# Performance work log

Measured on AMD Instinct MI355X. Metric: run time of the kernel, lower is better.

The kernel has to match this reference:

```python
import jax, jax.numpy as jnp
import numpy as np

EPS = 1e-8  # matches torch F.cosine_similarity eps


def setup_inputs() -> dict:
    key = jax.random.key(0)
    k1, = jax.random.split(key, 1)
    N, U, D = 512, 32, 512
    embeddings = jax.random.normal(k1, (N, U, D), dtype=jnp.float32)
    w = jnp.asarray(10.0, dtype=jnp.float32)  # init_w
    b = jnp.asarray(-5.0, dtype=jnp.float32)  # init_b
    return {"embeddings": embeddings, "w": w, "b": b}


def reference(embeddings, w, b):
    N, U, D = embeddings.shape
    # centroids per speaker (mean over utterances; module includes current utt)
    centroids = embeddings.mean(axis=1)  # (N, D)
    # cosine similarity via normalize + matmul
    e = embeddings.reshape(N * U, D)
    e_n = e / jnp.maximum(jnp.linalg.norm(e, axis=-1, keepdims=True), EPS)
    c_n = centroids / jnp.maximum(
        jnp.linalg.norm(centroids, axis=-1, keepdims=True), EPS)
    sim = (e_n @ c_n.T).reshape(N, U, N)  # (N, U, N)
    sim = w * sim + b
    logp = jax.nn.log_softmax(sim, axis=-1)  # (N, U, N)
    # pick logp[j, k, j] for every j, k
    diag = jnp.take_along_axis(
        logp, jnp.arange(N)[:, None, None], axis=2)[..., 0]  # (N, U)
    return -diag.mean()
```

## Files before the change

kernel.cpp:

```cpp
#include <hip/hip_runtime.h>
#include <math.h>

#define N_SPK 512
#define N_UTT 32
#define DIM   512
#define EPSN  1e-8f

typedef __attribute__((ext_vector_type(8))) short  short8;
typedef __attribute__((ext_vector_type(4))) float  f32x4;

__device__ inline unsigned short f2bf(float x) {
  unsigned int u = __builtin_bit_cast(unsigned int, x);
  unsigned int r = (u + 0x7fffu + ((u >> 16) & 1u)) >> 16;
  return (unsigned short)r;
}

#define CNK_ELEMS (N_SPK * DIM)

__global__ __launch_bounds__(256) void centroid_kernel(
    const float* __restrict__ emb, unsigned short* __restrict__ cnk) {
  int j = blockIdx.x, t = threadIdx.x;
  int c4 = t & 127, half = t >> 7;
  const float4* base = (const float4*)(emb + (size_t)j * N_UTT * DIM);
  float4 s = {0.f, 0.f, 0.f, 0.f};
#pragma unroll
  for (int u = 0; u < 16; ++u) {
    float4 v = base[(half + 2 * u) * 128 + c4];
    s.x += v.x; s.y += v.y; s.z += v.z; s.w += v.w;
  }
  __shared__ float4 comb[128];
  if (half) comb[c4] = s;
  __syncthreads();
  float4 m = {0.f, 0.f, 0.f, 0.f};
  float ss = 0.f;
  if (!half) {
    float4 o = comb[c4];
    m.x = (s.x + o.x) * (1.f / N_UTT);
    m.y = (s.y + o.y) * (1.f / N_UTT);
    m.z = (s.z + o.z) * (1.f / N_UTT);
    m.w = (s.w + o.w) * (1.f / N_UTT);
    ss = m.x * m.x + m.y * m.y + m.z * m.z + m.w * m.w;
  }
#pragma unroll
  for (int off = 32; off > 0; off >>= 1) ss += __shfl_xor(ss, off, 64);
  __shared__ float red[4];
  if ((t & 63) == 0) red[t >> 6] = ss;
  __syncthreads();
  float total = red[0] + red[1] + red[2] + red[3];
  float inv = 1.f / fmaxf(sqrtf(total), EPSN);
  if (!half) {
    int d0 = c4 * 4;
    int kc = d0 >> 5;
    unsigned short* p = cnk + ((size_t)kc * N_SPK + j) * 32 + (d0 & 31);
    p[0] = f2bf(m.x * inv); p[1] = f2bf(m.y * inv);
    p[2] = f2bf(m.z * inv); p[3] = f2bf(m.w * inv);
  }
}

__global__ __launch_bounds__(512, 4) void ge2e_kernel(
    const float* __restrict__ emb, const unsigned short* __restrict__ cnk,
    const float* __restrict__ wp, const float* __restrict__ bp,
    float* __restrict__ partials) {
  __shared__ __align__(16) unsigned short E[N_UTT * DIM];
  __shared__ float red[8][N_UTT][2];
  __shared__ float dred[8];

  int j = blockIdx.x;
  int t = threadIdx.x;
  int lane = t & 63, wid = t >> 6;
  int n15 = lane & 15, quad = lane >> 4;

#pragma unroll
  for (int r8 = 0; r8 < 4; ++r8) {
    int r = wid * 4 + r8;
    const float* rp = emb + ((size_t)j * N_UTT + r) * DIM + lane * 8;
    float4 v0 = *(const float4*)rp;
    float4 v1 = *(const float4*)(rp + 4);
    float ss = v0.x * v0.x + v0.y * v0.y + v0.z * v0.z + v0.w * v0.w +
               v1.x * v1.x + v1.y * v1.y + v1.z * v1.z + v1.w * v1.w;
#pragma unroll
    for (int off = 32; off > 0; off >>= 1) ss += __shfl_xor(ss, off, 64);
    float inv = 1.f / fmaxf(sqrtf(ss), EPSN);
    short8 pk;
    pk[0] = (short)f2bf(v0.x * inv); pk[1] = (short)f2bf(v0.y * inv);
    pk[2] = (short)f2bf(v0.z * inv); pk[3] = (short)f2bf(v0.w * inv);
    pk[4] = (short)f2bf(v1.x * inv); pk[5] = (short)f2bf(v1.y * inv);
    pk[6] = (short)f2bf(v1.z * inv); pk[7] = (short)f2bf(v1.w * inv);
    int sw = lane ^ (r & 7);
    *(short8*)&E[r * DIM + sw * 8] = pk;
  }
  __syncthreads();

  f32x4 acc[2][4];
#pragma unroll
  for (int mt = 0; mt < 2; ++mt)
#pragma unroll
    for (int nt = 0; nt < 4; ++nt) acc[mt][nt] = (f32x4){0.f, 0.f, 0.f, 0.f};

  for (int ks = 0; ks < 16; ++ks) {
    short8 b[4];
#pragma unroll
    for (int nt = 0; nt < 4; ++nt) {
      int c = wid * 64 + nt * 16 + n15;
      b[nt] = *(const short8*)(cnk + ((size_t)ks * N_SPK + c) * 32 + quad * 8);
    }
    short8 a[2];
#pragma unroll
    for (int mt = 0; mt < 2; ++mt) {
      int r = mt * 16 + n15;
      int sw = (ks * 4 + quad) ^ (r & 7);
      a[mt] = *(const short8*)&E[r * DIM + sw * 8];
    }
#pragma unroll
    for (int mt = 0; mt < 2; ++mt)
#pragma unroll
      for (int nt = 0; nt < 4; ++nt)
        acc[mt][nt] = __builtin_amdgcn_mfma_f32_16x16x32_bf16(
            a[mt], b[nt], acc[mt][nt], 0, 0, 0);
  }

  float w = *wp, bb = *bp;
  float dsum = 0.f;
#pragma unroll
  for (int mt = 0; mt < 2; ++mt)
#pragma unroll
    for (int nt = 0; nt < 4; ++nt) {
      int c = wid * 64 + nt * 16 + n15;
      bool isdiag = (c == j);
#pragma unroll
      for (int rg = 0; rg < 4; ++rg) {
        float v = fmaf(w, acc[mt][nt][rg], bb);
        acc[mt][nt][rg] = v;
        if (isdiag) dsum += v;
      }
    }

#pragma unroll
  for (int mt = 0; mt < 2; ++mt)
#pragma unroll
    for (int rg = 0; rg < 4; ++rg) {
      float m = -INFINITY;
#pragma unroll
      for (int nt = 0; nt < 4; ++nt) m = fmaxf(m, acc[mt][nt][rg]);
#pragma unroll
      for (int off = 1; off < 16; off <<= 1) m = fmaxf(m, __shfl_xor(m, off, 64));
      float s = 0.f;
#pragma unroll
      for (int nt = 0; nt < 4; ++nt) s += __expf(acc[mt][nt][rg] - m);
#pragma unroll
      for (int off = 1; off < 16; off <<= 1) s += __shfl_xor(s, off, 64);
      if (n15 == 0) {
        int r = mt * 16 + quad * 4 + rg;
        red[wid][r][0] = m;
        red[wid][r][1] = s;
      }
    }
#pragma unroll
  for (int off = 32; off > 0; off >>= 1) dsum += __shfl_xor(dsum, off, 64);
  if (lane == 0) dred[wid] = dsum;
  __syncthreads();

  if (t < 32) {
    float M = -INFINITY;
#pragma unroll
    for (int ww = 0; ww < 8; ++ww) M = fmaxf(M, red[ww][t][0]);
    float S = 0.f;
#pragma unroll
    for (int ww = 0; ww < 8; ++ww) S += red[ww][t][1] * __expf(red[ww][t][0] - M);
    float lse = M + __logf(S);
#pragma unroll
    for (int off = 16; off > 0; off >>= 1) lse += __shfl_xor(lse, off, 64);
    if (t == 0) {
      float d = dred[0] + dred[1] + dred[2] + dred[3] +
                dred[4] + dred[5] + dred[6] + dred[7];
      partials[j] = lse - d;
    }
  }
}

__global__ __launch_bounds__(512) void finalize_kernel(
    const float* __restrict__ partials, float* __restrict__ out) {
  int t = threadIdx.x;
  float v = partials[t];
#pragma unroll
  for (int off = 32; off > 0; off >>= 1) v += __shfl_xor(v, off, 64);
  __shared__ float r[8];
  if ((t & 63) == 0) r[t >> 6] = v;
  __syncthreads();
  if (t == 0) {
    float s = r[0] + r[1] + r[2] + r[3] + r[4] + r[5] + r[6] + r[7];
    out[0] = s * (1.f / (N_SPK * N_UTT));
  }
}

extern "C" void kernel_launch(void* const* d_in, const int* in_sizes, int n_in,
                              void* d_out, int out_size, void* d_ws, size_t ws_size,
                              hipStream_t stream) {
  const float* emb = (const float*)d_in[0];
  const float* wp  = (const float*)d_in[1];
  const float* bp  = (const float*)d_in[2];
  float* out = (float*)d_out;
  unsigned short* cnk = (unsigned short*)d_ws;
  float* partials = (float*)((char*)d_ws + (size_t)CNK_ELEMS * 2);

  centroid_kernel<<<N_SPK, 256, 0, stream>>>(emb, cnk);
  ge2e_kernel<<<N_SPK, 512, 0, stream>>>(emb, cnk, wp, bp, partials);
  finalize_kernel<<<1, 512, 0, stream>>>(partials, out);
}
```

Baseline: 98.80 us.

## Fuse centroid and similarity kernels into one cooperative kernel with grid sync

Replaces the separate centroid and GE2E kernels with one cooperative kernel of 256 blocks of 1024 threads, each handling two speakers. The centroids are computed from the embeddings already loaded for normalization, so the second global read of the embeddings and one launch go away, and a grid-wide sync is used before the matmul. Each block now computes a 64x512 tile, which reuses every centroid fragment over twice as many rows. The cost is grid-sync overhead and only 256 resident blocks, with a fallback to the old three-kernel path if the cooperative launch fails.

```diff
diff --git a/kernel.cpp b/kernel.cpp
--- a/kernel.cpp
+++ b/kernel.cpp
@@ -1,10 +1,15 @@
 #include <hip/hip_runtime.h>
+#include <hip/hip_cooperative_groups.h>
 #include <math.h>
+
+namespace cg = cooperative_groups;
 
 #define N_SPK 512
 #define N_UTT 32
 #define DIM   512
 #define EPSN  1e-8f
+#define NBLK  256
+#define NTHR  1024
 
 typedef __attribute__((ext_vector_type(8))) short  short8;
 typedef __attribute__((ext_vector_type(4))) float  f32x4;
@@ -16,6 +21,182 @@
 }
 
 #define CNK_ELEMS (N_SPK * DIM)
+
+__global__ __launch_bounds__(NTHR) void ge2e_fused(
+    const float* __restrict__ emb, unsigned short* __restrict__ cnk,
+    const float* __restrict__ wp, const float* __restrict__ bp,
+    float* __restrict__ partials) {
+  __shared__ __align__(16) unsigned short E[64 * DIM];
+  __shared__ __align__(16) float part[14][DIM];
+  __shared__ float red[16][64][2];
+  __shared__ float dred[16];
+
+  int b = blockIdx.x;
+  int t = threadIdx.x;
+  int lane = t & 63, wid = t >> 6;
+  int n15 = lane & 15, quad = lane >> 4;
+  int sp = wid >> 3, ws8 = wid & 7;
+  int j = 2 * b + sp;
+
+  float4 v0[4], v1[4];
+  const float* base = emb + ((size_t)j * N_UTT + ws8 * 4) * DIM + lane * 8;
+#pragma unroll
+  for (int r4 = 0; r4 < 4; ++r4) {
+    v0[r4] = *(const float4*)(base + r4 * DIM);
+    v1[r4] = *(const float4*)(base + r4 * DIM + 4);
+  }
+  float cen[8] = {0.f, 0.f, 0.f, 0.f, 0.f, 0.f, 0.f, 0.f};
+#pragma unroll
+  for (int r4 = 0; r4 < 4; ++r4) {
+    cen[0] += v0[r4].x; cen[1] += v0[r4].y; cen[2] += v0[r4].z; cen[3] += v0[r4].w;
+    cen[4] += v1[r4].x; cen[5] += v1[r4].y; cen[6] += v1[r4].z; cen[7] += v1[r4].w;
+    float ss = v0[r4].x * v0[r4].x + v0[r4].y * v0[r4].y +
+               v0[r4].z * v0[r4].z + v0[r4].w * v0[r4].w +
+               v1[r4].x * v1[r4].x + v1[r4].y * v1[r4].y +
+               v1[r4].z * v1[r4].z + v1[r4].w * v1[r4].w;
+#pragma unroll
+    for (int off = 32; off > 0; off >>= 1) ss += __shfl_xor(ss, off, 64);
+    float inv = 1.f / fmaxf(sqrtf(ss), EPSN);
+    short8 pk;
+    pk[0] = (short)f2bf(v0[r4].x * inv); pk[1] = (short)f2bf(v0[r4].y * inv);
+    pk[2] = (short)f2bf(v0[r4].z * inv); pk[3] = (short)f2bf(v0[r4].w * inv);
+    pk[4] = (short)f2bf(v1[r4].x * inv); pk[5] = (short)f2bf(v1[r4].y * inv);
+    pk[6] = (short)f2bf(v1[r4].z * inv); pk[7] = (short)f2bf(v1[r4].w * inv);
+    int R = sp * 32 + ws8 * 4 + r4;
+    int sw = lane ^ (R & 7);
+    *(short8*)&E[R * DIM + sw * 8] = pk;
+  }
+  if (ws8 != 0) {
+    float* p = &part[sp * 7 + ws8 - 1][lane * 8];
+    *(float4*)p       = (float4){cen[0], cen[1], cen[2], cen[3]};
+    *(float4*)(p + 4) = (float4){cen[4], cen[5], cen[6], cen[7]};
+  }
+  __syncthreads();
+  if (ws8 == 0) {
+#pragma unroll
+    for (int i = 0; i < 7; ++i) {
+      const float* p = &part[sp * 7 + i][lane * 8];
+      float4 a = *(const float4*)p, c = *(const float4*)(p + 4);
+      cen[0] += a.x; cen[1] += a.y; cen[2] += a.z; cen[3] += a.w;
+      cen[4] += c.x; cen[5] += c.y; cen[6] += c.z; cen[7] += c.w;
+    }
+    float ss = 0.f;
+#pragma unroll
+    for (int k = 0; k < 8; ++k) {
+      cen[k] *= (1.f / N_UTT);
+      ss += cen[k] * cen[k];
+    }
+#pragma unroll
+    for (int off = 32; off > 0; off >>= 1) ss += __shfl_xor(ss, off, 64);
+    float inv = 1.f / fmaxf(sqrtf(ss), EPSN);
+    int kc = lane >> 2, ko = (lane & 3) * 8;
+    short8 pk;
+#pragma unroll
+    for (int k = 0; k < 8; ++k) pk[k] = (short)f2bf(cen[k] * inv);
+    *(short8*)(cnk + ((size_t)kc * N_SPK + j) * 32 + ko) = pk;
+  }
+  __threadfence();
+  cg::this_grid().sync();
+
+  f32x4 acc[4][2];
+#pragma unroll
+  for (int mt = 0; mt < 4; ++mt)
+#pragma unroll
+    for (int nt = 0; nt < 2; ++nt) acc[mt][nt] = (f32x4){0.f, 0.f, 0.f, 0.f};
+
+#pragma unroll 4
+  for (int ks = 0; ks < 16; ++ks) {
+    short8 bfr[2];
+#pragma unroll
+    for (int nt = 0; nt < 2; ++nt) {
+      int c = wid * 32 + nt * 16 + n15;
+      bfr[nt] = *(const short8*)(cnk + ((size_t)ks * N_SPK + c) * 32 + quad * 8);
+    }
+    short8 afr[4];
+#pragma unroll
+    for (int mt = 0; mt < 4; ++mt) {
+      int r = mt * 16 + n15;
+      int sw = (ks * 4 + quad) ^ (r & 7);
+      afr[mt] = *(const short8*)&E[r * DIM + sw * 8];
+    }
+#pragma unroll
+    for (int mt = 0; mt < 4; ++mt)
+#pragma unroll
+      for (int nt = 0; nt < 2; ++nt)
+        acc[mt][nt] = __builtin_amdgcn_mfma_f32_16x16x32_bf16(
+            afr[mt], bfr[nt], acc[mt][nt], 0, 0, 0);
+  }
+
+  float w = *wp, bb = *bp;
+  float dsum = 0.f;
+#pragma unroll
+  for (int mt = 0; mt < 4; ++mt)
+#pragma unroll
+    for (int nt = 0; nt < 2; ++nt) {
+      int c = wid * 32 + nt * 16 + n15;
+      bool isdiag = (c == 2 * b + (mt >> 1));
+#pragma unroll
+      for (int rg = 0; rg < 4; ++rg) {
+        float v = fmaf(w, acc[mt][nt][rg], bb);
+        acc[mt][nt][rg] = v;
+        if (isdiag) dsum += v;
+      }
+    }
+
+#pragma unroll
+  for (int mt = 0; mt < 4; ++mt)
+#pragma unroll
+    for (int rg = 0; rg < 4; ++rg) {
+      float m = fmaxf(acc[mt][0][rg], acc[mt][1][rg]);
+#pragma unroll
+      for (int off = 1; off < 16; off <<= 1) m = fmaxf(m, __shfl_xor(m, off, 64));
+      float s = __expf(acc[mt][0][rg] - m) + __expf(acc[mt][1][rg] - m);
+#pragma unroll
+      for (int off = 1; off < 16; off <<= 1) s += __shfl_xor(s, off, 64);
+      if (n15 == 0) {
+        int r = mt * 16 + quad * 4 + rg;
+        red[wid][r][0] = m;
+        red[wid][r][1] = s;
+      }
+    }
+#pragma unroll
+  for (int off = 32; off > 0; off >>= 1) dsum += __shfl_xor(dsum, off, 64);
+  if (lane == 0) dred[wid] = dsum;
+  __syncthreads();
+
+  if (t < 64) {
+    float M = -INFINITY;
+#pragma unroll
+    for (int ww = 0; ww < 16; ++ww) M = fmaxf(M, red[ww][t][0]);
+    float S = 0.f;
+#pragma unroll
+    for (int ww = 0; ww < 16; ++ww) S += red[ww][t][1] * __expf(red[ww][t][0] - M);
+    float lse = M + __logf(S);
+#pragma unroll
+    for (int off = 32; off > 0; off >>= 1) lse += __shfl_xor(lse, off, 64);
+    if (t == 0) {
+      float d = 0.f;
+#pragma unroll
+      for (int ww = 0; ww < 16; ++ww) d += dred[ww];
+      partials[b] = lse - d;
+    }
+  }
+}
+
+__global__ __launch_bounds__(512) void finalize_kernel(
+    const float* __restrict__ partials, float* __restrict__ out, int n) {
+  int t = threadIdx.x;
+  float v = (t < n) ? partials[t] : 0.f;
+#pragma unroll
+  for (int off = 32; off > 0; off >>= 1) v += __shfl_xor(v, off, 64);
+  __shared__ float r[8];
+  if ((t & 63) == 0) r[t >> 6] = v;
+  __syncthreads();
+  if (t == 0) {
+    float s = r[0] + r[1] + r[2] + r[3] + r[4] + r[5] + r[6] + r[7];
+    out[0] = s * (1.f / (N_SPK * N_UTT));
+  }
+}
 
 __global__ __launch_bounds__(256) void centroid_kernel(
     const float* __restrict__ emb, unsigned short* __restrict__ cnk) {
@@ -98,25 +279,25 @@
     for (int nt = 0; nt < 4; ++nt) acc[mt][nt] = (f32x4){0.f, 0.f, 0.f, 0.f};
 
   for (int ks = 0; ks < 16; ++ks) {
-    short8 b[4];
+    short8 bf[4];
 #pragma unroll
     for (int nt = 0; nt < 4; ++nt) {
       int c = wid * 64 + nt * 16 + n15;
-      b[nt] = *(const short8*)(cnk + ((size_t)ks * N_SPK + c) * 32 + quad * 8);
-    }
-    short8 a[2];
+      bf[nt] = *(const short8*)(cnk + ((size_t)ks * N_SPK + c) * 32 + quad * 8);
+    }
+    short8 af[2];
 #pragma unroll
     for (int mt = 0; mt < 2; ++mt) {
       int r = mt * 16 + n15;
       int sw = (ks * 4 + quad) ^ (r & 7);
-      a[mt] = *(const short8*)&E[r * DIM + sw * 8];
+      af[mt] = *(const short8*)&E[r * DIM + sw * 8];
     }
 #pragma unroll
     for (int mt = 0; mt < 2; ++mt)
 #pragma unroll
       for (int nt = 0; nt < 4; ++nt)
         acc[mt][nt] = __builtin_amdgcn_mfma_f32_16x16x32_bf16(
-            a[mt], b[nt], acc[mt][nt], 0, 0, 0);
+            af[mt], bf[nt], acc[mt][nt], 0, 0, 0);
   }
 
   float w = *wp, bb = *bp;
@@ -175,21 +356,6 @@
                 dred[4] + dred[5] + dred[6] + dred[7];
       partials[j] = lse - d;
     }
-  }
-}
-
-__global__ __launch_bounds__(512) void finalize_kernel(
-    const float* __restrict__ partials, float* __restrict__ out) {
-  int t = threadIdx.x;
-  float v = partials[t];
-#pragma unroll
-  for (int off = 32; off > 0; off >>= 1) v += __shfl_xor(v, off, 64);
-  __shared__ float r[8];
-  if ((t & 63) == 0) r[t >> 6] = v;
-  __syncthreads();
-  if (t == 0) {
-    float s = r[0] + r[1] + r[2] + r[3] + r[4] + r[5] + r[6] + r[7];
-    out[0] = s * (1.f / (N_SPK * N_UTT));
   }
 }
 
@@ -203,7 +369,15 @@
   unsigned short* cnk = (unsigned short*)d_ws;
   float* partials = (float*)((char*)d_ws + (size_t)CNK_ELEMS * 2);
 
-  centroid_kernel<<<N_SPK, 256, 0, stream>>>(emb, cnk);
-  ge2e_kernel<<<N_SPK, 512, 0, stream>>>(emb, cnk, wp, bp, partials);
-  finalize_kernel<<<1, 512, 0, stream>>>(partials, out);
-}
+  void* args[] = {(void*)&emb, (void*)&cnk, (void*)&wp, (void*)&bp,
+                  (void*)&partials};
+  hipError_t err = hipLaunchCooperativeKernel(
+      (const void*)ge2e_fused, dim3(NBLK), dim3(NTHR), args, 0, stream);
+  if (err == hipSuccess) {
+    finalize_kernel<<<1, 512, 0, stream>>>(partials, out, NBLK);
+  } else {
+    centroid_kernel<<<N_SPK, 256, 0, stream>>>(emb, cnk);
+    ge2e_kernel<<<N_SPK, 512, 0, stream>>>(emb, cnk, wp, bp, partials);
+    finalize_kernel<<<1, 512, 0, stream>>>(partials, out, N_SPK);
+  }
+}
```

New measurement: 193.9 us. +96.3%, slower.

## Process two speakers per block to halve centroid fragment reloads

Applied to the files above, without the earlier changes.

Each ge2e block now handles two speakers (64 rows) with 1024 threads, and every wave covers 32 centroid columns and 4 row tiles instead of 64 columns and 2 row tiles. Each centroid fragment loaded from global memory is reused across twice as many rows, so total centroid traffic drops by half. The trade-off is 256 blocks instead of 512, which on a large GPU may leave compute units idle, plus twice the LDS per block, which lowers occupancy. The finalize kernel is shrunk to match the 256 partials.

```diff
diff --git a/kernel.cpp b/kernel.cpp
--- a/kernel.cpp
+++ b/kernel.cpp
@@ -57,23 +57,25 @@
   }
 }
 
-__global__ __launch_bounds__(512, 4) void ge2e_kernel(
+__global__ __launch_bounds__(1024) void ge2e_kernel(
     const float* __restrict__ emb, const unsigned short* __restrict__ cnk,
     const float* __restrict__ wp, const float* __restrict__ bp,
     float* __restrict__ partials) {
-  __shared__ __align__(16) unsigned short E[N_UTT * DIM];
-  __shared__ float red[8][N_UTT][2];
-  __shared__ float dred[8];
-
-  int j = blockIdx.x;
+  __shared__ __align__(16) unsigned short E[64 * DIM];
+  __shared__ float red[16][64][2];
+  __shared__ float dred[16];
+
+  int b = blockIdx.x;
   int t = threadIdx.x;
   int lane = t & 63, wid = t >> 6;
   int n15 = lane & 15, quad = lane >> 4;
-
-#pragma unroll
-  for (int r8 = 0; r8 < 4; ++r8) {
-    int r = wid * 4 + r8;
-    const float* rp = emb + ((size_t)j * N_UTT + r) * DIM + lane * 8;
+  int sp = wid >> 3, ws8 = wid & 7;
+  int j = 2 * b + sp;
+
+#pragma unroll
+  for (int r4 = 0; r4 < 4; ++r4) {
+    int R = sp * 32 + ws8 * 4 + r4;
+    const float* rp = emb + ((size_t)j * N_UTT + ws8 * 4 + r4) * DIM + lane * 8;
     float4 v0 = *(const float4*)rp;
     float4 v1 = *(const float4*)(rp + 4);
     float ss = v0.x * v0.x + v0.y * v0.y + v0.z * v0.z + v0.w * v0.w +
@@ -86,47 +88,47 @@
     pk[2] = (short)f2bf(v0.z * inv); pk[3] = (short)f2bf(v0.w * inv);
     pk[4] = (short)f2bf(v1.x * inv); pk[5] = (short)f2bf(v1.y * inv);
     pk[6] = (short)f2bf(v1.z * inv); pk[7] = (short)f2bf(v1.w * inv);
-    int sw = lane ^ (r & 7);
-    *(short8*)&E[r * DIM + sw * 8] = pk;
-  }
-  __syncthreads();
-
-  f32x4 acc[2][4];
-#pragma unroll
-  for (int mt = 0; mt < 2; ++mt)
-#pragma unroll
-    for (int nt = 0; nt < 4; ++nt) acc[mt][nt] = (f32x4){0.f, 0.f, 0.f, 0.f};
+    int sw = lane ^ (R & 7);
+    *(short8*)&E[R * DIM + sw * 8] = pk;
+  }
+  __syncthreads();
+
+  f32x4 acc[4][2];
+#pragma unroll
+  for (int mt = 0; mt < 4; ++mt)
+#pragma unroll
+    for (int nt = 0; nt < 2; ++nt) acc[mt][nt] = (f32x4){0.f, 0.f, 0.f, 0.f};
 
   for (int ks = 0; ks < 16; ++ks) {
-    short8 b[4];
-#pragma unroll
-    for (int nt = 0; nt < 4; ++nt) {
-      int c = wid * 64 + nt * 16 + n15;
-      b[nt] = *(const short8*)(cnk + ((size_t)ks * N_SPK + c) * 32 + quad * 8);
-    }
-    short8 a[2];
-#pragma unroll
-    for (int mt = 0; mt < 2; ++mt) {
+    short8 bfr[2];
+#pragma unroll
+    for (int nt = 0; nt < 2; ++nt) {
+      int c = wid * 32 + nt * 16 + n15;
+      bfr[nt] = *(const short8*)(cnk + ((size_t)ks * N_SPK + c) * 32 + quad * 8);
+    }
+    short8 afr[4];
+#pragma unroll
+    for (int mt = 0; mt < 4; ++mt) {
       int r = mt * 16 + n15;
       int sw = (ks * 4 + quad) ^ (r & 7);
-      a[mt] = *(const short8*)&E[r * DIM + sw * 8];
-    }
-#pragma unroll
-    for (int mt = 0; mt < 2; ++mt)
-#pragma unroll
-      for (int nt = 0; nt < 4; ++nt)
+      afr[mt] = *(const short8*)&E[r * DIM + sw * 8];
+    }
+#pragma unroll
+    for (int mt = 0; mt < 4; ++mt)
+#pragma unroll
+      for (int nt = 0; nt < 2; ++nt)
         acc[mt][nt] = __builtin_amdgcn_mfma_f32_16x16x32_bf16(
-            a[mt], b[nt], acc[mt][nt], 0, 0, 0);
+            afr[mt], bfr[nt], acc[mt][nt], 0, 0, 0);
   }
 
   float w = *wp, bb = *bp;
   float dsum = 0.f;
 #pragma unroll
-  for (int mt = 0; mt < 2; ++mt)
-#pragma unroll
-    for (int nt = 0; nt < 4; ++nt) {
-      int c = wid * 64 + nt * 16 + n15;
-      bool isdiag = (c == j);
+  for (int mt = 0; mt < 4; ++mt)
+#pragma unroll
+    for (int nt = 0; nt < 2; ++nt) {
+      int c = wid * 32 + nt * 16 + n15;
+      bool isdiag = (c == 2 * b + (mt >> 1));
 #pragma unroll
       for (int rg = 0; rg < 4; ++rg) {
         float v = fmaf(w, acc[mt][nt][rg], bb);
@@ -136,17 +138,13 @@
     }
 
 #pragma unroll
-  for (int mt = 0; mt < 2; ++mt)
+  for (int mt = 0; mt < 4; ++mt)
 #pragma unroll
     for (int rg = 0; rg < 4; ++rg) {
-      float m = -INFINITY;
-#pragma unroll
-      for (int nt = 0; nt < 4; ++nt) m = fmaxf(m, acc[mt][nt][rg]);
+      float m = fmaxf(acc[mt][0][rg], acc[mt][1][rg]);
 #pragma unroll
       for (int off = 1; off < 16; off <<= 1) m = fmaxf(m, __shfl_xor(m, off, 64));
-      float s = 0.f;
-#pragma unroll
-      for (int nt = 0; nt < 4; ++nt) s += __expf(acc[mt][nt][rg] - m);
+      float s = __expf(acc[mt][0][rg] - m) + __expf(acc[mt][1][rg] - m);
 #pragma unroll
       for (int off = 1; off < 16; off <<= 1) s += __shfl_xor(s, off, 64);
       if (n15 == 0) {
@@ -160,35 +158,36 @@
   if (lane == 0) dred[wid] = dsum;
   __syncthreads();
 
-  if (t < 32) {
+  if (t < 64) {
     float M = -INFINITY;
 #pragma unroll
-    for (int ww = 0; ww < 8; ++ww) M = fmaxf(M, red[ww][t][0]);
+    for (int ww = 0; ww < 16; ++ww) M = fmaxf(M, red[ww][t][0]);
     float S = 0.f;
 #pragma unroll
-    for (int ww = 0; ww < 8; ++ww) S += red[ww][t][1] * __expf(red[ww][t][0] - M);
+    for (int ww = 0; ww < 16; ++ww) S += red[ww][t][1] * __expf(red[ww][t][0] - M);
     float lse = M + __logf(S);
 #pragma unroll
-    for (int off = 16; off > 0; off >>= 1) lse += __shfl_xor(lse, off, 64);
+    for (int off = 32; off > 0; off >>= 1) lse += __shfl_xor(lse, off, 64);
     if (t == 0) {
-      float d = dred[0] + dred[1] + dred[2] + dred[3] +
-                dred[4] + dred[5] + dred[6] + dred[7];
-      partials[j] = lse - d;
-    }
-  }
-}
-
-__global__ __launch_bounds__(512) void finalize_kernel(
+      float d = 0.f;
+#pragma unroll
+      for (int ww = 0; ww < 16; ++ww) d += dred[ww];
+      partials[b] = lse - d;
+    }
+  }
+}
+
+__global__ __launch_bounds__(256) void finalize_kernel(
     const float* __restrict__ partials, float* __restrict__ out) {
   int t = threadIdx.x;
   float v = partials[t];
 #pragma unroll
   for (int off = 32; off > 0; off >>= 1) v += __shfl_xor(v, off, 64);
-  __shared__ float r[8];
+  __shared__ float r[4];
   if ((t & 63) == 0) r[t >> 6] = v;
   __syncthreads();
   if (t == 0) {
-    float s = r[0] + r[1] + r[2] + r[3] + r[4] + r[5] + r[6] + r[7];
+    float s = r[0] + r[1] + r[2] + r[3];
     out[0] = s * (1.f / (N_SPK * N_UTT));
   }
 }
@@ -204,6 +203,6 @@
   float* partials = (float*)((char*)d_ws + (size_t)CNK_ELEMS * 2);
 
   centroid_kernel<<<N_SPK, 256, 0, stream>>>(emb, cnk);
-  ge2e_kernel<<<N_SPK, 512, 0, stream>>>(emb, cnk, wp, bp, partials);
-  finalize_kernel<<<1, 512, 0, stream>>>(partials, out);
-}
+  ge2e_kernel<<<256, 1024, 0, stream>>>(emb, cnk, wp, bp, partials);
+  finalize_kernel<<<1, 256, 0, stream>>>(partials, out);
+}
```

Measured after the change: 99.06 us. Within noise of the previous version (+0.3%).
